# Kernel optimization log

Measured on AMD Instinct MI355X. Metric: run time of the kernel, lower is better.

## Reference

```python
import jax, jax.numpy as jnp
import numpy as np

NUM_HEADS = 16


def setup_inputs() -> dict:
    key = jax.random.key(0)
    ks = jax.random.split(key, 5)
    bs, seq, d_in, hidden = 2, 2048, 1024, 1024
    s = 0.02
    return {
        "x": jax.random.normal(ks[0], (bs, seq, d_in), jnp.float32),
        "Wq": jax.random.normal(ks[1], (hidden, d_in), jnp.float32) * s,
        "bq": jnp.zeros((hidden,), jnp.float32),
        "Wk": jax.random.normal(ks[2], (hidden, d_in), jnp.float32) * s,
        "bk": jnp.zeros((hidden,), jnp.float32),
        "Wv": jax.random.normal(ks[3], (hidden, d_in), jnp.float32) * s,
        "bv": jnp.zeros((hidden,), jnp.float32),
        "Wm": jax.random.normal(ks[4], (hidden, hidden), jnp.float32) * s,
        "bm": jnp.zeros((hidden,), jnp.float32),
    }


def reference(x, Wq, bq, Wk, bk, Wv, bv, Wm, bm):
    bs, seq, _ = x.shape
    hidden = Wq.shape[0]
    H = NUM_HEADS
    d = hidden // H
    scale = d ** 0.5
    # Linear projections (torch nn.Linear: x @ W.T + b), split into heads.
    # torch code splits last dim then cats along batch; equivalent to a
    # [bs, seq, H, d] reshape with head-major last-dim blocks.
    q = (x @ Wq.T + bq).reshape(bs, seq, H, d)
    k = (x @ Wk.T + bk).reshape(bs, seq, H, d)
    v = (x @ Wv.T + bv).reshape(bs, seq, H, d)
    scores = jnp.einsum("bqhd,bkhd->bhqk", q, k) / scale  # [bs,H,seq,seq]
    causal = jnp.tril(jnp.ones((seq, seq), bool))
    scores = jnp.where(causal, scores, -jnp.inf)
    probs = jax.nn.softmax(scores, axis=-1)
    att = jnp.einsum("bhqk,bkhd->bqhd", probs, v).reshape(bs, seq, hidden)
    return att @ Wm.T + bm
```

## Files before the change

### kernel.cpp

```cpp
#include <hip/hip_runtime.h>
#include <hip/hip_bf16.h>
#include <cstdint>
#include <cstddef>

typedef unsigned short u16;
typedef short s8v __attribute__((ext_vector_type(8)));
typedef float f4v __attribute__((ext_vector_type(4)));
typedef float f16v __attribute__((ext_vector_type(16)));

#define SEQ   2048
#define BSZ   2
#define HID   1024
#define NH    16
#define DH    64
#define MROWS (BSZ*SEQ)
#define CLOG  0.18033688011112042f
#define THR2  6.0f

__device__ __forceinline__ u16 f2b(float x) {
  union { float f; uint32_t u; } c; c.f = x;
  uint32_t r = (c.u + 0x7fffu + ((c.u >> 16) & 1u)) >> 16;
  return (u16)r;
}
__device__ __forceinline__ float b2f(u16 v) {
  union { uint32_t u; float f; } c; c.u = (uint32_t)v << 16;
  return c.f;
}

__device__ __forceinline__ f4v mfma16(s8v a, s8v b, f4v c) {
  return __builtin_amdgcn_mfma_f32_16x16x32_bf16(a, b, c, 0, 0, 0);
}
__device__ __forceinline__ f16v mfma32(s8v a, s8v b, f16v c) {
  return __builtin_amdgcn_mfma_f32_32x32x16_bf16(a, b, c, 0, 0, 0);
}

__device__ __forceinline__ float fexp2(float x) {
#if __has_builtin(__builtin_amdgcn_exp2f)
  return __builtin_amdgcn_exp2f(x);
#else
  return exp2f(x);
#endif
}

__device__ __forceinline__ uint32_t pkbf16(float a, float b) {
  uint32_t d;
  asm("v_cvt_pk_bf16_f32 %0, %1, %2" : "=v"(d) : "v"(a), "v"(b));
  return d;
}
__device__ __forceinline__ void pswap(uint32_t& x, uint32_t& y) {
  asm("v_permlane32_swap_b32 %0, %1" : "+v"(x), "+v"(y));
}

typedef __attribute__((address_space(1))) const void gas_void;
typedef __attribute__((address_space(3))) void las_void;
__device__ __forceinline__ void gload_lds16(const void* g, void* l) {
  __builtin_amdgcn_global_load_lds((gas_void*)g, (las_void*)l, 16, 0, 0);
}

__global__ __launch_bounds__(256) void cvt5(
    const float* __restrict__ s0, const float* __restrict__ s1,
    const float* __restrict__ s2, const float* __restrict__ s3,
    const float* __restrict__ s4,
    u16* __restrict__ d0, u16* __restrict__ d1, u16* __restrict__ d2,
    u16* __restrict__ d3, u16* __restrict__ d4)
{
  const float* s; u16* d; int n;
  switch (blockIdx.y) {
    case 0:  s = s0; d = d0; n = MROWS*HID; break;
    case 1:  s = s1; d = d1; n = HID*HID;   break;
    case 2:  s = s2; d = d2; n = HID*HID;   break;
    case 3:  s = s3; d = d3; n = HID*HID;   break;
    default: s = s4; d = d4; n = HID*HID;   break;
  }
  const int n8 = n >> 3;
  const int stride = gridDim.x * blockDim.x;
  for (int i = blockIdx.x * blockDim.x + threadIdx.x; i < n8; i += stride) {
    const float4* p = (const float4*)s + (size_t)i * 2;
    float4 a = p[0], b = p[1];
    s8v ov;
    ov[0] = (short)f2b(a.x); ov[1] = (short)f2b(a.y);
    ov[2] = (short)f2b(a.z); ov[3] = (short)f2b(a.w);
    ov[4] = (short)f2b(b.x); ov[5] = (short)f2b(b.y);
    ov[6] = (short)f2b(b.z); ov[7] = (short)f2b(b.w);
    ((s8v*)d)[i] = ov;
  }
}

__global__ __launch_bounds__(256) void gemm_qkv(
    const u16* __restrict__ A,
    const u16* __restrict__ B0, const u16* __restrict__ B1, const u16* __restrict__ B2,
    const float* __restrict__ bias0, const float* __restrict__ bias1, const float* __restrict__ bias2,
    const float sc0, const float sc1, const float sc2,
    void* C0, void* C1, void* C2,
    const int Ksz)
{
  const u16* Bp; const float* bias; void* Cp; float sc;
  if (blockIdx.z == 0)      { Bp = B0; bias = bias0; Cp = C0; sc = sc0; }
  else if (blockIdx.z == 1) { Bp = B1; bias = bias1; Cp = C1; sc = sc1; }
  else                      { Bp = B2; bias = bias2; Cp = C2; sc = sc2; }

  __shared__ __align__(16) u16 As[128 * 64];
  __shared__ __align__(16) u16 Bs[128 * 64];

  const int t  = threadIdx.x;
  const int w  = t >> 6;
  const int l  = t & 63;
  const int lr = l & 15;
  const int lg = l >> 4;
  const int wr = w >> 1;
  const int wc = w & 1;

  const int bm = blockIdx.x, bn = blockIdx.y;

  const int srow = t >> 3;
  const int scol = (t & 7) * 8;

  const u16* gA = A  + (size_t)(bm * 128 + srow) * Ksz + scol;
  const u16* gB = Bp + (size_t)(bn * 128 + srow) * Ksz + scol;
  const size_t ck = (size_t)32 * Ksz;

  const f4v fzero = {0.f, 0.f, 0.f, 0.f};
  f4v acc[4][4];
#pragma unroll
  for (int m = 0; m < 4; ++m)
#pragma unroll
    for (int n = 0; n < 4; ++n) acc[m][n] = fzero;

  const int nk = Ksz >> 6;
  for (int kt = 0; kt < nk; ++kt) {
    if (kt) __syncthreads();
    gload_lds16(gA,          &As[t * 8]);
    gload_lds16(gA + ck,     &As[2048 + t * 8]);
    gload_lds16(gA + 2 * ck, &As[4096 + t * 8]);
    gload_lds16(gA + 3 * ck, &As[6144 + t * 8]);
    gload_lds16(gB,          &Bs[t * 8]);
    gload_lds16(gB + ck,     &Bs[2048 + t * 8]);
    gload_lds16(gB + 2 * ck, &Bs[4096 + t * 8]);
    gload_lds16(gB + 3 * ck, &Bs[6144 + t * 8]);
    gA += 64; gB += 64;
    __syncthreads();

#pragma unroll
    for (int kk = 0; kk < 2; ++kk) {
      s8v af[4], bfr[4];
#pragma unroll
      for (int m = 0; m < 4; ++m)
        af[m] = *(const s8v*)&As[(wr * 64 + m * 16 + lr) * 64 + kk * 32 + lg * 8];
#pragma unroll
      for (int n = 0; n < 4; ++n)
        bfr[n] = *(const s8v*)&Bs[(wc * 64 + n * 16 + lr) * 64 + kk * 32 + lg * 8];
#pragma unroll
      for (int m = 0; m < 4; ++m)
#pragma unroll
        for (int n = 0; n < 4; ++n)
          acc[m][n] = mfma16(af[m], bfr[n], acc[m][n]);
    }
  }

  if (blockIdx.z == 1) {
#pragma unroll
    for (int n = 0; n < 4; ++n) {
      const int col = bn * 128 + wc * 64 + n * 16 + lr;
      const float bv = bias[col];
      const int h  = col >> 6;
      const int d6 = col & 63;
      const int j  = d6 >> 4;
      const int hic = (d6 >> 3) & 1;
      const int e  = d6 & 7;
#pragma unroll
      for (int m = 0; m < 4; ++m) {
#pragma unroll
        for (int r = 0; r < 4; ++r) {
          const int row = bm * 128 + wr * 64 + m * 16 + lg * 4 + r;
          const int bb = row >> 11;
          const int s  = row & (SEQ - 1);
          const int tile = s >> 5;
          const int l31r = s & 31;
          const size_t idx = ((((size_t)(bb * NH + h) * 64 + tile) * 4 + j) * 512)
                           + (size_t)hic * 256 + (size_t)l31r * 8 + e;
          ((u16*)Cp)[idx] = f2b((acc[m][n][r] + bv) * sc);
        }
      }
    }
  } else if (blockIdx.z == 2) {
#pragma unroll
    for (int n = 0; n < 4; ++n) {
      const int col = bn * 128 + wc * 64 + n * 16 + lr;
      const float bv = bias[col];
      const int h    = col >> 6;
      const int dt   = (col >> 5) & 1;
      const int l31c = col & 31;
#pragma unroll
      for (int m = 0; m < 4; ++m) {
        const int row0 = bm * 128 + wr * 64 + m * 16 + lg * 4;
        const int bb = row0 >> 11;
        const int s0 = row0 & (SEQ - 1);
        const int tile = s0 >> 5;
        const int u    = (s0 >> 4) & 1;
        const int hiw  = (s0 >> 3) & 1;
        const int e0   = s0 & 7;
        const size_t idx = ((((size_t)(bb * NH + h) * 64 + tile) * 2 + u) * 2 + dt) * 512
                         + (size_t)hiw * 256 + (size_t)l31c * 8 + e0;
        ushort4 pk;
        pk.x = f2b((acc[m][n][0] + bv) * sc);
        pk.y = f2b((acc[m][n][1] + bv) * sc);
        pk.z = f2b((acc[m][n][2] + bv) * sc);
        pk.w = f2b((acc[m][n][3] + bv) * sc);
        *(ushort4*)((u16*)Cp + idx) = pk;
      }
    }
  } else {
#pragma unroll
    for (int n = 0; n < 4; ++n) {
      const int col = bn * 128 + wc * 64 + n * 16 + lr;
      const float bv = bias[col];
#pragma unroll
      for (int m = 0; m < 4; ++m) {
#pragma unroll
        for (int r = 0; r < 4; ++r) {
          const int row = bm * 128 + wr * 64 + m * 16 + lg * 4 + r;
          ((u16*)Cp)[(size_t)row * HID + col] = f2b((acc[m][n][r] + bv) * sc);
        }
      }
    }
  }
}

__global__ __launch_bounds__(256) void gemm_out(
    const u16* __restrict__ A, const u16* __restrict__ B,
    const float* __restrict__ bias, float* __restrict__ C, const int Ksz, const int Nsz)
{
  __shared__ __align__(16) u16 As[64 * 32];
  __shared__ __align__(16) u16 Bs[64 * 32];

  const int t  = threadIdx.x;
  const int w  = t >> 6;
  const int l  = t & 63;
  const int lr = l & 15;
  const int lg = l >> 4;
  const int wr = w >> 1;
  const int wc = w & 1;

  const int bm = blockIdx.x, bn = blockIdx.y;

  const int srow = t >> 2;
  const int scol = (t & 3) * 8;

  const u16* gA = A + (size_t)(bm * 64 + srow) * Ksz + scol;
  const u16* gB = B + (size_t)(bn * 64 + srow) * Ksz + scol;

  const f4v fzero = {0.f, 0.f, 0.f, 0.f};
  f4v acc[2][2];
#pragma unroll
  for (int m = 0; m < 2; ++m)
#pragma unroll
    for (int n = 0; n < 2; ++n) acc[m][n] = fzero;

  const int nk = Ksz >> 5;
  for (int kt = 0; kt < nk; ++kt) {
    if (kt) __syncthreads();
    gload_lds16(gA, &As[t * 8]);
    gload_lds16(gB, &Bs[t * 8]);
    gA += 32; gB += 32;
    __syncthreads();

    s8v af[2], bfr[2];
#pragma unroll
    for (int m = 0; m < 2; ++m)
      af[m] = *(const s8v*)&As[(wr * 32 + m * 16 + lr) * 32 + lg * 8];
#pragma unroll
    for (int n = 0; n < 2; ++n)
      bfr[n] = *(const s8v*)&Bs[(wc * 32 + n * 16 + lr) * 32 + lg * 8];
#pragma unroll
    for (int m = 0; m < 2; ++m)
#pragma unroll
      for (int n = 0; n < 2; ++n)
        acc[m][n] = mfma16(af[m], bfr[n], acc[m][n]);
  }

#pragma unroll
  for (int n = 0; n < 2; ++n) {
    const int col = bn * 64 + wc * 32 + n * 16 + lr;
    const float bv = bias[col];
#pragma unroll
    for (int m = 0; m < 2; ++m) {
#pragma unroll
      for (int r = 0; r < 4; ++r) {
        const int row = bm * 64 + wr * 32 + m * 16 + lg * 4 + r;
        C[(size_t)row * Nsz + col] = acc[m][n][r] + bv;
      }
    }
  }
}

__global__ __launch_bounds__(256, 4) void attn_fused(
    const u16* __restrict__ Qm, const u16* __restrict__ Kp,
    const u16* __restrict__ Vp, u16* __restrict__ Om)
{
  __shared__ __align__(16) u16 Oaccb[4 * 32 * 66];
  __shared__ float Msh[4][32];
  __shared__ float Lsh[4][32];
  __shared__ float Rsh[4][32];

  const int h  = blockIdx.x;
  const int b  = blockIdx.y;
  const int pz = blockIdx.z;
  const int t  = threadIdx.x;
  const int w  = t >> 6;
  const int l  = t & 63;
  const int l31 = l & 31;
  const int hi  = l >> 5;
  const int hi8 = hi * 8;
  const int hi4 = hi * 4;

  const u16* Qb = Qm + (size_t)(b * SEQ) * HID + h * DH;
  const u16* Kpb = Kp + (size_t)(b * NH + h) * 64 * 2048 + (size_t)l * 8;
  const u16* Vpb = Vp + (size_t)(b * NH + h) * 64 * 2048 + (size_t)l * 8;

  const f16v z16 = {0.f,0.f,0.f,0.f,0.f,0.f,0.f,0.f,0.f,0.f,0.f,0.f,0.f,0.f,0.f,0.f};

  for (int pi = 0; pi < 2; ++pi) {
    const int qt  = pi ? (63 - pz) : pz;
    const int qr0 = qt * 32;

    const u16* qrow = Qb + (size_t)(qr0 + l31) * HID + hi8;
    const s8v q0 = *(const s8v*)(qrow);
    const s8v q1 = *(const s8v*)(qrow + 16);
    const s8v q2 = *(const s8v*)(qrow + 32);
    const s8v q3 = *(const s8v*)(qrow + 48);

    f16v o0 = z16, o1 = z16;
    float mrow = -1e30f, lrow = 0.f;

    for (int kt = w; kt <= qt; kt += 4) {
      const u16* ktb = Kpb + (size_t)kt * 2048;
      const s8v ak0 = *(const s8v*)(ktb);
      const s8v ak1 = *(const s8v*)(ktb + 512);
      const s8v ak2 = *(const s8v*)(ktb + 1024);
      const s8v ak3 = *(const s8v*)(ktb + 1536);
      const u16* vtb = Vpb + (size_t)kt * 2048;
      const s8v bv00 = *(const s8v*)(vtb);
      const s8v bv01 = *(const s8v*)(vtb + 512);
      const s8v bv10 = *(const s8v*)(vtb + 1024);
      const s8v bv11 = *(const s8v*)(vtb + 1536);

      f16v st = z16;
      __builtin_amdgcn_s_setprio(1);
      st = mfma32(ak0, q0, st);
      st = mfma32(ak1, q1, st);
      st = mfma32(ak2, q2, st);
      st = mfma32(ak3, q3, st);
      __builtin_amdgcn_s_setprio(0);

      if (kt == qt) {
#pragma unroll
        for (int r = 0; r < 16; ++r)
          if (((r & 3) + 8 * (r >> 2) + hi4) > l31) st[r] = -1e30f;
      }

      float a0 = fmaxf(st[0], st[8]),  a1 = fmaxf(st[1], st[9]);
      float a2 = fmaxf(st[2], st[10]), a3 = fmaxf(st[3], st[11]);
      float a4 = fmaxf(st[4], st[12]), a5 = fmaxf(st[5], st[13]);
      float a6 = fmaxf(st[6], st[14]), a7 = fmaxf(st[7], st[15]);
      float b0 = fmaxf(a0, a4), b1 = fmaxf(a1, a5), b2 = fmaxf(a2, a6), b3 = fmaxf(a3, a7);
      float tm = fmaxf(fmaxf(b0, b1), fmaxf(b2, b3));
      tm = fmaxf(tm, __shfl_xor(tm, 32, 64));

      if (!__all((tm - mrow <= THR2) ? 1 : 0)) {
        const float mn = fmaxf(mrow, tm);
        const float rs = fexp2(mrow - mn);
        mrow = mn;
        lrow *= rs;
        if (l < 32) Rsh[w][l31] = rs;
#pragma unroll
        for (int r = 0; r < 16; ++r) {
          const float f = Rsh[w][(r & 3) + 8 * (r >> 2) + hi4];
          o0[r] *= f; o1[r] *= f;
        }
      }

      float p[16];
#pragma unroll
      for (int r = 0; r < 16; ++r) p[r] = fexp2(st[r] - mrow);

      float u0 = p[0]+p[8],  u1 = p[1]+p[9],  u2 = p[2]+p[10], u3 = p[3]+p[11];
      float u4 = p[4]+p[12], u5 = p[5]+p[13], u6 = p[6]+p[14], u7 = p[7]+p[15];
      float v0 = u0+u4, v1 = u1+u5, v2 = u2+u6, v3 = u3+u7;
      float ts = (v0+v1) + (v2+v3);
      ts += __shfl_xor(ts, 32, 64);
      lrow += ts;

      uint32_t A0 = pkbf16(p[0], p[1]),  A1 = pkbf16(p[2], p[3]);
      uint32_t B0 = pkbf16(p[4], p[5]),  B1 = pkbf16(p[6], p[7]);
      pswap(A0, B0); pswap(A1, B1);
      uint32_t C0 = pkbf16(p[8], p[9]),  C1 = pkbf16(p[10], p[11]);
      uint32_t D0 = pkbf16(p[12], p[13]), D1 = pkbf16(p[14], p[15]);
      pswap(C0, D0); pswap(C1, D1);
      union { uint32_t wd[4]; s8v v; } f0, f1;
      f0.wd[0] = A0; f0.wd[1] = A1; f0.wd[2] = B0; f0.wd[3] = B1;
      f1.wd[0] = C0; f1.wd[1] = C1; f1.wd[2] = D0; f1.wd[3] = D1;

      __builtin_amdgcn_s_setprio(1);
      o0 = mfma32(f0.v, bv00, o0);
      o0 = mfma32(f1.v, bv10, o0);
      o1 = mfma32(f0.v, bv01, o1);
      o1 = mfma32(f1.v, bv11, o1);
      __builtin_amdgcn_s_setprio(0);
    }

    if (l < 32) { Msh[w][l31] = mrow; Lsh[w][l31] = lrow; }
    __syncthreads();

    float fr[16];
#pragma unroll
    for (int r = 0; r < 16; ++r) {
      const int q = (r & 3) + 8 * (r >> 2) + hi4;
      float M = fmaxf(fmaxf(Msh[0][q], Msh[1][q]), fmaxf(Msh[2][q], Msh[3][q]));
      fr[r] = fexp2(Msh[w][q] - M);
    }
#pragma unroll
    for (int r = 0; r < 16; ++r) {
      const int q = (r & 3) + 8 * (r >> 2) + hi4;
      Oaccb[(w * 32 + q) * 66 + l31]      = f2b(o0[r] * fr[r]);
      Oaccb[(w * 32 + q) * 66 + 33 + l31] = f2b(o1[r] * fr[r]);
    }
    __syncthreads();

#pragma unroll
    for (int j = 0; j < 8; ++j) {
      const int row = w * 8 + j;
      float M = fmaxf(fmaxf(Msh[0][row], Msh[1][row]), fmaxf(Msh[2][row], Msh[3][row]));
      float lt = 0.f;
#pragma unroll
      for (int wp = 0; wp < 4; ++wp) lt += fexp2(Msh[wp][row] - M) * Lsh[wp][row];
      const int cof = (l >= 32) ? (33 + l31) : l31;
      float v = 0.f;
#pragma unroll
      for (int wp = 0; wp < 4; ++wp) v += b2f(Oaccb[(wp * 32 + row) * 66 + cof]);
      Om[(size_t)(b * SEQ + qr0 + row) * HID + h * DH + l] = f2b(v / lt);
    }
    __syncthreads();
  }
}

extern "C" void kernel_launch(void* const* d_in, const int* in_sizes, int n_in,
                              void* d_out, int out_size, void* d_ws, size_t ws_size,
                              hipStream_t stream) {
  const float* x  = (const float*)d_in[0];
  const float* Wq = (const float*)d_in[1];
  const float* bq = (const float*)d_in[2];
  const float* Wk = (const float*)d_in[3];
  const float* bk = (const float*)d_in[4];
  const float* Wv = (const float*)d_in[5];
  const float* bv = (const float*)d_in[6];
  const float* Wm = (const float*)d_in[7];
  const float* bm = (const float*)d_in[8];
  float* out = (float*)d_out;

  u16* xb  = (u16*)d_ws;
  u16* Wqb = xb  + (size_t)MROWS * HID;
  u16* Wkb = Wqb + (size_t)HID * HID;
  u16* Wvb = Wkb + (size_t)HID * HID;
  u16* Wmb = Wvb + (size_t)HID * HID;
  u16* Qm  = Wmb + (size_t)HID * HID;
  u16* Kp  = Qm  + (size_t)MROWS * HID;
  u16* Vp  = Kp  + (size_t)MROWS * HID;
  u16* att = Vp  + (size_t)MROWS * HID;

  cvt5<<<dim3(512, 5, 1), 256, 0, stream>>>(x, Wq, Wk, Wv, Wm, xb, Wqb, Wkb, Wvb, Wmb);
  gemm_qkv<<<dim3(32, 8, 3), 256, 0, stream>>>(
      xb, Wqb, Wkb, Wvb, bq, bk, bv, CLOG, 1.f, 1.f, Qm, Kp, Vp, HID);
  attn_fused<<<dim3(16, 2, 32), 256, 0, stream>>>(Qm, Kp, Vp, att);
  gemm_out<<<dim3(64, 16), 256, 0, stream>>>(att, Wmb, bm, out, HID, HID);
}
```

Measured before the change: 116.8 us.

## Shrink QKV GEMM tiles, swizzle workgroup order, use fragment-native LDS layout

The QKV projection GEMM drops from 128x128 tiles with K=64 steps to 128x64 tiles with K=32 steps, doubling the grid and cutting LDS and accumulator use. Both GEMMs remap the linear workgroup id with an XCD-aware swizzle so neighbouring tiles land on the same chiplet and share L2. Global-to-LDS loads are rearranged so each wave's 16x32 MFMA fragment sits contiguously in LDS, letting fragments be read as l*8 with no bank conflicts. The cost is less operand reuse per tile and more k-loop iterations and barriers.

```diff
diff --git a/kernel.cpp b/kernel.cpp
--- a/kernel.cpp
+++ b/kernel.cpp
@@ -94,13 +94,20 @@
     void* C0, void* C1, void* C2,
     const int Ksz)
 {
+  const int wgid = blockIdx.x + 32 * (blockIdx.y + 16 * blockIdx.z);
+  const int swz  = (wgid & 7) * 192 + (wgid >> 3);
+  const int bm   = swz / 48;
+  const int rem  = swz % 48;
+  const int bn   = rem / 3;
+  const int z    = rem % 3;
+
   const u16* Bp; const float* bias; void* Cp; float sc;
-  if (blockIdx.z == 0)      { Bp = B0; bias = bias0; Cp = C0; sc = sc0; }
-  else if (blockIdx.z == 1) { Bp = B1; bias = bias1; Cp = C1; sc = sc1; }
-  else                      { Bp = B2; bias = bias2; Cp = C2; sc = sc2; }
-
-  __shared__ __align__(16) u16 As[128 * 64];
-  __shared__ __align__(16) u16 Bs[128 * 64];
+  if (z == 0)      { Bp = B0; bias = bias0; Cp = C0; sc = sc0; }
+  else if (z == 1) { Bp = B1; bias = bias1; Cp = C1; sc = sc1; }
+  else             { Bp = B2; bias = bias2; Cp = C2; sc = sc2; }
+
+  __shared__ __align__(16) u16 As[8 * 512];
+  __shared__ __align__(16) u16 Bs[4 * 512];
 
   const int t  = threadIdx.x;
   const int w  = t >> 6;
@@ -110,57 +117,47 @@
   const int wr = w >> 1;
   const int wc = w & 1;
 
-  const int bm = blockIdx.x, bn = blockIdx.y;
-
-  const int srow = t >> 3;
-  const int scol = (t & 7) * 8;
-
-  const u16* gA = A  + (size_t)(bm * 128 + srow) * Ksz + scol;
-  const u16* gB = Bp + (size_t)(bn * 128 + srow) * Ksz + scol;
-  const size_t ck = (size_t)32 * Ksz;
+  const int arow = ((t >> 6) << 4) + (t & 15);
+  const int acol = ((t >> 4) & 3) * 8;
+
+  const u16* gA = A  + (size_t)(bm * 128 + arow) * Ksz + acol;
+  const u16* gB = Bp + (size_t)(bn * 64  + arow) * Ksz + acol;
+  const size_t half = (size_t)64 * Ksz;
 
   const f4v fzero = {0.f, 0.f, 0.f, 0.f};
-  f4v acc[4][4];
+  f4v acc[4][2];
 #pragma unroll
   for (int m = 0; m < 4; ++m)
 #pragma unroll
-    for (int n = 0; n < 4; ++n) acc[m][n] = fzero;
-
-  const int nk = Ksz >> 6;
+    for (int n = 0; n < 2; ++n) acc[m][n] = fzero;
+
+  const int nk = Ksz >> 5;
   for (int kt = 0; kt < nk; ++kt) {
     if (kt) __syncthreads();
-    gload_lds16(gA,          &As[t * 8]);
-    gload_lds16(gA + ck,     &As[2048 + t * 8]);
-    gload_lds16(gA + 2 * ck, &As[4096 + t * 8]);
-    gload_lds16(gA + 3 * ck, &As[6144 + t * 8]);
-    gload_lds16(gB,          &Bs[t * 8]);
-    gload_lds16(gB + ck,     &Bs[2048 + t * 8]);
-    gload_lds16(gB + 2 * ck, &Bs[4096 + t * 8]);
-    gload_lds16(gB + 3 * ck, &Bs[6144 + t * 8]);
-    gA += 64; gB += 64;
+    gload_lds16(gA,        &As[t * 8]);
+    gload_lds16(gA + half, &As[2048 + t * 8]);
+    gload_lds16(gB,        &Bs[t * 8]);
+    gA += 32; gB += 32;
     __syncthreads();
 
-#pragma unroll
-    for (int kk = 0; kk < 2; ++kk) {
-      s8v af[4], bfr[4];
-#pragma unroll
-      for (int m = 0; m < 4; ++m)
-        af[m] = *(const s8v*)&As[(wr * 64 + m * 16 + lr) * 64 + kk * 32 + lg * 8];
-#pragma unroll
-      for (int n = 0; n < 4; ++n)
-        bfr[n] = *(const s8v*)&Bs[(wc * 64 + n * 16 + lr) * 64 + kk * 32 + lg * 8];
-#pragma unroll
-      for (int m = 0; m < 4; ++m)
-#pragma unroll
-        for (int n = 0; n < 4; ++n)
-          acc[m][n] = mfma16(af[m], bfr[n], acc[m][n]);
-    }
-  }
-
-  if (blockIdx.z == 1) {
-#pragma unroll
-    for (int n = 0; n < 4; ++n) {
-      const int col = bn * 128 + wc * 64 + n * 16 + lr;
+    s8v af[4], bfr[2];
+#pragma unroll
+    for (int m = 0; m < 4; ++m)
+      af[m] = *(const s8v*)&As[(wr * 4 + m) * 512 + l * 8];
+#pragma unroll
+    for (int n = 0; n < 2; ++n)
+      bfr[n] = *(const s8v*)&Bs[(wc * 2 + n) * 512 + l * 8];
+#pragma unroll
+    for (int m = 0; m < 4; ++m)
+#pragma unroll
+      for (int n = 0; n < 2; ++n)
+        acc[m][n] = mfma16(af[m], bfr[n], acc[m][n]);
+  }
+
+  if (z == 1) {
+#pragma unroll
+    for (int n = 0; n < 2; ++n) {
+      const int col = bn * 64 + wc * 32 + n * 16 + lr;
       const float bv = bias[col];
       const int h  = col >> 6;
       const int d6 = col & 63;
@@ -182,10 +179,10 @@
         }
       }
     }
-  } else if (blockIdx.z == 2) {
-#pragma unroll
-    for (int n = 0; n < 4; ++n) {
-      const int col = bn * 128 + wc * 64 + n * 16 + lr;
+  } else if (z == 2) {
+#pragma unroll
+    for (int n = 0; n < 2; ++n) {
+      const int col = bn * 64 + wc * 32 + n * 16 + lr;
       const float bv = bias[col];
       const int h    = col >> 6;
       const int dt   = (col >> 5) & 1;
@@ -211,8 +208,8 @@
     }
   } else {
 #pragma unroll
-    for (int n = 0; n < 4; ++n) {
-      const int col = bn * 128 + wc * 64 + n * 16 + lr;
+    for (int n = 0; n < 2; ++n) {
+      const int col = bn * 64 + wc * 32 + n * 16 + lr;
       const float bv = bias[col];
 #pragma unroll
       for (int m = 0; m < 4; ++m) {
@@ -230,8 +227,13 @@
     const u16* __restrict__ A, const u16* __restrict__ B,
     const float* __restrict__ bias, float* __restrict__ C, const int Ksz, const int Nsz)
 {
-  __shared__ __align__(16) u16 As[64 * 32];
-  __shared__ __align__(16) u16 Bs[64 * 32];
+  const int wgid = blockIdx.x + 64 * blockIdx.y;
+  const int swz  = (wgid & 7) * 128 + (wgid >> 3);
+  const int bm   = swz >> 4;
+  const int bn   = swz & 15;
+
+  __shared__ __align__(16) u16 As[4 * 512];
+  __shared__ __align__(16) u16 Bs[4 * 512];
 
   const int t  = threadIdx.x;
   const int w  = t >> 6;
@@ -241,13 +243,11 @@
   const int wr = w >> 1;
   const int wc = w & 1;
 
-  const int bm = blockIdx.x, bn = blockIdx.y;
-
-  const int srow = t >> 2;
-  const int scol = (t & 3) * 8;
-
-  const u16* gA = A + (size_t)(bm * 64 + srow) * Ksz + scol;
-  const u16* gB = B + (size_t)(bn * 64 + srow) * Ksz + scol;
+  const int arow = ((t >> 6) << 4) + (t & 15);
+  const int acol = ((t >> 4) & 3) * 8;
+
+  const u16* gA = A + (size_t)(bm * 64 + arow) * Ksz + acol;
+  const u16* gB = B + (size_t)(bn * 64 + arow) * Ksz + acol;
 
   const f4v fzero = {0.f, 0.f, 0.f, 0.f};
   f4v acc[2][2];
@@ -267,10 +267,10 @@
     s8v af[2], bfr[2];
 #pragma unroll
     for (int m = 0; m < 2; ++m)
-      af[m] = *(const s8v*)&As[(wr * 32 + m * 16 + lr) * 32 + lg * 8];
+      af[m] = *(const s8v*)&As[(wr * 2 + m) * 512 + l * 8];
 #pragma unroll
     for (int n = 0; n < 2; ++n)
-      bfr[n] = *(const s8v*)&Bs[(wc * 32 + n * 16 + lr) * 32 + lg * 8];
+      bfr[n] = *(const s8v*)&Bs[(wc * 2 + n) * 512 + l * 8];
 #pragma unroll
     for (int m = 0; m < 2; ++m)
 #pragma unroll
@@ -468,7 +468,7 @@
   u16* att = Vp  + (size_t)MROWS * HID;
 
   cvt5<<<dim3(512, 5, 1), 256, 0, stream>>>(x, Wq, Wk, Wv, Wm, xb, Wqb, Wkb, Wvb, Wmb);
-  gemm_qkv<<<dim3(32, 8, 3), 256, 0, stream>>>(
+  gemm_qkv<<<dim3(32, 16, 3), 256, 0, stream>>>(
       xb, Wqb, Wkb, Wvb, bq, bk, bv, CLOG, 1.f, 1.f, Qm, Kp, Vp, HID);
   attn_fused<<<dim3(16, 2, 32), 256, 0, stream>>>(Qm, Kp, Vp, att);
   gemm_out<<<dim3(64, 16), 256, 0, stream>>>(att, Wmb, bm, out, HID, HID);
```

After: 162.1 us. 1.39x slower.
